# Kernel optimization log

Measured on AMD Instinct MI355X. Metric: run time of the kernel, lower is better.

## Reference

```python
import jax, jax.numpy as jnp
import numpy as np

N_NODES = 100_000
N_EDGES = 20_000   # hyperedges
NNZ = 2_000_000    # incidence pairs
F = 128
BN_EPS = 1e-5


def setup_inputs() -> dict:
    key = jax.random.key(0)
    ks = jax.random.split(key, 6)
    x_0 = jax.random.normal(ks[0], (N_NODES, F), dtype=jnp.float32)
    x_1 = jax.random.normal(ks[1], (N_EDGES, F), dtype=jnp.float32)
    node_idx = jax.random.randint(ks[2], (NNZ,), 0, N_NODES, dtype=jnp.int32)
    edge_idx = jax.random.randint(ks[3], (NNZ,), 0, N_EDGES, dtype=jnp.int32)
    W_nh = jax.random.normal(ks[4], (F, F), dtype=jnp.float32) / np.float32(np.sqrt(F))
    b_nh = jnp.zeros((F,), jnp.float32)
    W_en = jax.random.normal(ks[5], (F, 2 * F), dtype=jnp.float32) / np.float32(np.sqrt(2 * F))
    b_en = jnp.zeros((F,), jnp.float32)
    ones = jnp.ones((F,), jnp.float32)
    zeros = jnp.zeros((F,), jnp.float32)
    return {
        "x_0": x_0, "x_1": x_1, "node_idx": node_idx, "edge_idx": edge_idx,
        "W_nh": W_nh, "b_nh": b_nh, "W_en": W_en, "b_en": b_en,
        "bn0_gamma": ones, "bn0_beta": zeros, "bn0_mean": zeros, "bn0_var": ones,
        "bn1_gamma": ones, "bn1_beta": zeros, "bn1_mean": zeros, "bn1_var": ones,
    }


def _bn_eval(x, gamma, beta, mean, var):
    # BatchNorm1d in eval mode: normalize with running stats.
    return (x - mean) * (gamma * jax.lax.rsqrt(var + BN_EPS)) + beta


def reference(x_0, x_1, node_idx, edge_idx, W_nh, b_nh, W_en, b_en,
              bn0_gamma, bn0_beta, bn0_mean, bn0_var,
              bn1_gamma, bn1_beta, bn1_mean, bn1_var):
    # --- node -> hyperedge messenger ---
    # per-node message: sigmoid(Linear(x_0))  [n_nodes, F]
    node_messages = jax.nn.sigmoid(x_0 @ W_nh.T + b_nh)
    # gather over incidence list, scatter-sum onto hyperedges  [n_edges, F]
    node_msg_agg = jax.ops.segment_sum(node_messages[node_idx], edge_idx,
                                       num_segments=N_EDGES)

    # --- hyperedge -> node messenger ---
    # per-hyperedge message: sigmoid(Linear(cat(x_1, agg node msgs)))  [n_edges, F]
    he_messages = jax.nn.sigmoid(
        jnp.concatenate([x_1, node_msg_agg], axis=1) @ W_en.T + b_en)
    # gather per incidence, scatter-sum onto nodes  [n_nodes, F]
    he_msg_agg = jax.ops.segment_sum(he_messages[edge_idx], node_idx,
                                     num_segments=N_NODES)

    # --- updates (eval mode: feature dropout is identity) ---
    x0_out = jax.nn.sigmoid(
        _bn_eval(x_0, bn0_gamma, bn0_beta, bn0_mean, bn0_var) + he_msg_agg)
    x1_out = jax.nn.sigmoid(
        _bn_eval(x_1, bn1_gamma, bn1_beta, bn1_mean, bn1_var) + node_msg_agg)
    return (x0_out, x1_out)
```

## Files before the change

### kernel.cpp

```cpp
#include <hip/hip_runtime.h>
#include <hip/hip_bf16.h>
#include <math.h>

#define NNODES 100000
#define NEDGES 20000
#define NNZ_   2000000
#define FDIM   128
#define BN_EPS 1e-5f

#define NBUCK 256
#define CAP   9216
#define BPB_E 79
#define BPB_N 391
#define SH_E  17
#define SH_N  15

__device__ __forceinline__ float sigmoidf_(float x) {
    return 1.0f / (1.0f + __expf(-x));
}
__device__ __forceinline__ float bf2f(unsigned short u) {
    return __uint_as_float(((unsigned)u) << 16);
}
__device__ __forceinline__ unsigned short f2bf(float f) {
    __hip_bfloat16 h = __float2bfloat16(f);
    return *reinterpret_cast<unsigned short*>(&h);
}

__global__ __launch_bounds__(256) void transpose2(
    const float* __restrict__ W_nh, const float* __restrict__ W_en,
    float* __restrict__ WTnh, float* __restrict__ WTen)
{
    int idx = blockIdx.x * blockDim.x + threadIdx.x;
    if (idx < FDIM * FDIM) {
        int k = idx >> 7, c = idx & 127;
        WTnh[idx] = W_nh[c * FDIM + k];
    } else {
        int j = idx - FDIM * FDIM;
        if (j >= 2 * FDIM * FDIM) return;
        int k = j >> 7, c = j & 127;
        WTen[j] = W_en[c * 2 * FDIM + k];
    }
}

template<int K>
__global__ __launch_bounds__(256, 2) void gemm_sig_bf16(
    const float* __restrict__ A1, const float* __restrict__ A2,
    const float* __restrict__ WT, const float* __restrict__ bias,
    unsigned short* __restrict__ out)
{
    constexpr int BK = 64;
    constexpr int TM = 32;
    __shared__ float As[TM][BK + 4];
    __shared__ float Ws[BK][FDIM];
    const int tid  = threadIdx.x;
    const int row0 = blockIdx.x * TM;
    const int tcol = tid & 31;
    const int trow = tid >> 5;
    float acc[4][4] = {};

    for (int kk = 0; kk < K; kk += BK) {
        const float* Asrc = (kk < FDIM) ? A1 : A2;
        const int koff    = (kk < FDIM) ? kk : kk - FDIM;
        #pragma unroll
        for (int i = 0; i < 2; i++) {
            int l = tid + i * 256;
            int r = l >> 4, j = l & 15;
            float4 v = *(const float4*)(Asrc + (size_t)(row0 + r) * FDIM + koff + j * 4);
            *(float4*)&As[r][j * 4] = v;
        }
        #pragma unroll
        for (int i = 0; i < 8; i++) {
            int l = tid + i * 256;
            int k = l >> 5, j = l & 31;
            float4 v = *(const float4*)(WT + (size_t)(kk + k) * FDIM + j * 4);
            *(float4*)&Ws[k][j * 4] = v;
        }
        __syncthreads();
        #pragma unroll
        for (int k = 0; k < BK; k += 4) {
            float4 a[4];
            #pragma unroll
            for (int r = 0; r < 4; r++)
                a[r] = *(const float4*)&As[trow * 4 + r][k];
            #pragma unroll
            for (int kq = 0; kq < 4; kq++) {
                float4 w = *(const float4*)&Ws[k + kq][tcol * 4];
                #pragma unroll
                for (int r = 0; r < 4; r++) {
                    float av = (kq == 0) ? a[r].x : (kq == 1) ? a[r].y
                             : (kq == 2) ? a[r].z : a[r].w;
                    acc[r][0] += av * w.x;
                    acc[r][1] += av * w.y;
                    acc[r][2] += av * w.z;
                    acc[r][3] += av * w.w;
                }
            }
        }
        __syncthreads();
    }
    float4 bv = *(const float4*)(bias + tcol * 4);
    #pragma unroll
    for (int r = 0; r < 4; r++) {
        int row = row0 + trow * 4 + r;
        ushort4 o;
        o.x = f2bf(sigmoidf_(acc[r][0] + bv.x));
        o.y = f2bf(sigmoidf_(acc[r][1] + bv.y));
        o.z = f2bf(sigmoidf_(acc[r][2] + bv.z));
        o.w = f2bf(sigmoidf_(acc[r][3] + bv.w));
        *(ushort4*)(out + (size_t)row * FDIM + tcol * 4) = o;
    }
}

__global__ __launch_bounds__(1024) void bucket_scatter(
    const int* __restrict__ ni, const int* __restrict__ ei,
    unsigned* __restrict__ buck_e, unsigned* __restrict__ buck_n,
    int* __restrict__ gcur_e, int* __restrict__ gcur_n)
{
    __shared__ int lh_e[NBUCK], lh_n[NBUCK], lb_e[NBUCK], lb_n[NBUCK];
    const int t = threadIdx.x;
    if (t < NBUCK) { lh_e[t] = 0; lh_n[t] = 0; }
    __syncthreads();
    unsigned ent_e[4], ent_n[4];
    int be[4], bn[4], re[4], rn[4];
    const int base = blockIdx.x * 4096;
    #pragma unroll
    for (int j = 0; j < 4; j++) {
        int i = base + j * 1024 + t;
        if (i < NNZ_) {
            unsigned n = (unsigned)ni[i], e = (unsigned)ei[i];
            ent_e[j] = (e << SH_E) | n;  be[j] = (int)(e / BPB_E);
            ent_n[j] = (n << SH_N) | e;  bn[j] = (int)(n / BPB_N);
            re[j] = atomicAdd(&lh_e[be[j]], 1);
            rn[j] = atomicAdd(&lh_n[bn[j]], 1);
        } else { be[j] = -1; }
    }
    __syncthreads();
    if (t < NBUCK) {
        lb_e[t] = t * CAP + atomicAdd(&gcur_e[t], lh_e[t]);
        lb_n[t] = t * CAP + atomicAdd(&gcur_n[t], lh_n[t]);
    }
    __syncthreads();
    #pragma unroll
    for (int j = 0; j < 4; j++) {
        if (be[j] >= 0) {
            buck_e[(size_t)lb_e[be[j]] + re[j]] = ent_e[j];
            buck_n[(size_t)lb_n[bn[j]] + rn[j]] = ent_n[j];
        }
    }
}

__global__ __launch_bounds__(256) void bucket_bases(
    const int* __restrict__ gcur_e, const int* __restrict__ gcur_n,
    int* __restrict__ base_e, int* __restrict__ base_n)
{
    __shared__ int sh[NBUCK];
    int t = threadIdx.x;
    int v = gcur_e[t]; sh[t] = v; __syncthreads();
    for (int d = 1; d < NBUCK; d <<= 1) {
        int u = (t >= d) ? sh[t - d] : 0; __syncthreads();
        sh[t] += u; __syncthreads();
    }
    base_e[t] = sh[t] - v; __syncthreads();
    int v2 = gcur_n[t]; sh[t] = v2; __syncthreads();
    for (int d = 1; d < NBUCK; d <<= 1) {
        int u = (t >= d) ? sh[t - d] : 0; __syncthreads();
        sh[t] += u; __syncthreads();
    }
    base_n[t] = sh[t] - v2;
}

template<int BPB, int SH, unsigned MASK, int NBINS, typename OUT>
__device__ __forceinline__ void sort_bucket(
    const unsigned* __restrict__ region, int cnt, int gbase, int b0,
    OUT* __restrict__ csr, int* __restrict__ off)
{
    __shared__ unsigned lh[512];
    __shared__ unsigned lw[4];
    const int t = threadIdx.x;
    lh[t] = 0; lh[t + 256] = 0;
    __syncthreads();
    for (int i = t; i < cnt; i += 256) {
        int bin = (int)(region[i] >> SH) - b0;
        atomicAdd(&lh[bin], 1u);
    }
    __syncthreads();
    unsigned h0 = lh[2 * t], h1 = lh[2 * t + 1];
    unsigned s = h0 + h1, inc = s;
    const int lane = t & 63;
    #pragma unroll
    for (int d = 1; d <= 32; d <<= 1) {
        unsigned v = (unsigned)__shfl_up((int)inc, d, 64);
        if (lane >= d) inc += v;
    }
    if (lane == 63) lw[t >> 6] = inc;
    __syncthreads();
    unsigned pre = 0;
    #pragma unroll
    for (int w = 0; w < 4; w++) if (w < (t >> 6)) pre += lw[w];
    unsigned excl = pre + inc - s;
    unsigned c0 = (unsigned)gbase + excl;
    unsigned c1 = c0 + h0;
    lh[2 * t] = c0; lh[2 * t + 1] = c1;
    int i0 = 2 * t, i1 = 2 * t + 1;
    if (i0 <= BPB && b0 + i0 <= NBINS) off[b0 + i0] = (int)c0;
    if (i1 <= BPB && b0 + i1 <= NBINS) off[b0 + i1] = (int)c1;
    __syncthreads();
    for (int i = t; i < cnt; i += 256) {
        unsigned ent = region[i];
        int bin = (int)(ent >> SH) - b0;
        unsigned pos = atomicAdd(&lh[bin], 1u);
        csr[pos] = (OUT)(ent & MASK);
    }
}

__global__ __launch_bounds__(256) void bucket_sort(
    const unsigned* __restrict__ buck_e, const unsigned* __restrict__ buck_n,
    const int* __restrict__ gcur_e, const int* __restrict__ gcur_n,
    const int* __restrict__ base_e, const int* __restrict__ base_n,
    unsigned* __restrict__ csr_e, unsigned short* __restrict__ csr_n,
    int* __restrict__ off_e, int* __restrict__ off_n)
{
    int b = blockIdx.x & 255;
    if (blockIdx.x < 256)
        sort_bucket<BPB_E, SH_E, 0x1FFFFu, NEDGES, unsigned>(
            buck_e + (size_t)b * CAP, gcur_e[b], base_e[b], b * BPB_E, csr_e, off_e);
    else
        sort_bucket<BPB_N, SH_N, 0x7FFFu, NNODES, unsigned short>(
            buck_n + (size_t)b * CAP, gcur_n[b], base_n[b], b * BPB_N, csr_n, off_n);
}

template<typename IDX>
__global__ __launch_bounds__(256) void seg_sum_fin_bf16(
    const unsigned short* __restrict__ table, const IDX* __restrict__ csr,
    const int* __restrict__ off, const float* __restrict__ x,
    const float* __restrict__ g, const float* __restrict__ bb,
    const float* __restrict__ mm, const float* __restrict__ vv,
    float* __restrict__ agg_out, float* __restrict__ fin_out, int nseg)
{
    int gid = blockIdx.x * blockDim.x + threadIdx.x;
    int seg = gid >> 5;
    if (seg >= nseg) return;
    int q = (gid & 31) * 4;
    int i0 = off[seg], i1 = off[seg + 1];
    float4 acc = make_float4(0.f, 0.f, 0.f, 0.f);
    int i = i0;
    for (; i + 3 < i1; i += 4) {
        int r0 = (int)csr[i], r1 = (int)csr[i + 1];
        int r2 = (int)csr[i + 2], r3 = (int)csr[i + 3];
        ushort4 a0 = *(const ushort4*)(table + (size_t)r0 * FDIM + q);
        ushort4 a1 = *(const ushort4*)(table + (size_t)r1 * FDIM + q);
        ushort4 a2 = *(const ushort4*)(table + (size_t)r2 * FDIM + q);
        ushort4 a3 = *(const ushort4*)(table + (size_t)r3 * FDIM + q);
        acc.x += (bf2f(a0.x) + bf2f(a1.x)) + (bf2f(a2.x) + bf2f(a3.x));
        acc.y += (bf2f(a0.y) + bf2f(a1.y)) + (bf2f(a2.y) + bf2f(a3.y));
        acc.z += (bf2f(a0.z) + bf2f(a1.z)) + (bf2f(a2.z) + bf2f(a3.z));
        acc.w += (bf2f(a0.w) + bf2f(a1.w)) + (bf2f(a2.w) + bf2f(a3.w));
    }
    for (; i < i1; i++) {
        int r = (int)csr[i];
        ushort4 a = *(const ushort4*)(table + (size_t)r * FDIM + q);
        acc.x += bf2f(a.x); acc.y += bf2f(a.y);
        acc.z += bf2f(a.z); acc.w += bf2f(a.w);
    }
    if (agg_out)
        *(float4*)(agg_out + (size_t)seg * FDIM + q) = acc;
    if (fin_out) {
        float4 xv = *(const float4*)(x + (size_t)seg * FDIM + q);
        float4 gg = *(const float4*)(g + q);
        float4 bt = *(const float4*)(bb + q);
        float4 mn = *(const float4*)(mm + q);
        float4 vr = *(const float4*)(vv + q);
        float4 o;
        o.x = sigmoidf_((xv.x - mn.x) * (gg.x * rsqrtf(vr.x + BN_EPS)) + bt.x + acc.x);
        o.y = sigmoidf_((xv.y - mn.y) * (gg.y * rsqrtf(vr.y + BN_EPS)) + bt.y + acc.y);
        o.z = sigmoidf_((xv.z - mn.z) * (gg.z * rsqrtf(vr.z + BN_EPS)) + bt.z + acc.z);
        o.w = sigmoidf_((xv.w - mn.w) * (gg.w * rsqrtf(vr.w + BN_EPS)) + bt.w + acc.w);
        *(float4*)(fin_out + (size_t)seg * FDIM + q) = o;
    }
}

extern "C" void kernel_launch(void* const* d_in, const int* in_sizes, int n_in,
                              void* d_out, int out_size, void* d_ws, size_t ws_size,
                              hipStream_t stream)
{
    const float* x0       = (const float*)d_in[0];
    const float* x1       = (const float*)d_in[1];
    const int*   node_idx = (const int*)d_in[2];
    const int*   edge_idx = (const int*)d_in[3];
    const float* W_nh     = (const float*)d_in[4];
    const float* b_nh     = (const float*)d_in[5];
    const float* W_en     = (const float*)d_in[6];
    const float* b_en     = (const float*)d_in[7];
    const float* bn0g = (const float*)d_in[8];
    const float* bn0b = (const float*)d_in[9];
    const float* bn0m = (const float*)d_in[10];
    const float* bn0v = (const float*)d_in[11];
    const float* bn1g = (const float*)d_in[12];
    const float* bn1b = (const float*)d_in[13];
    const float* bn1m = (const float*)d_in[14];
    const float* bn1v = (const float*)d_in[15];

    float* ws = (float*)d_ws;
    float* B    = ws;
    float* WTnh = B + (size_t)NEDGES * FDIM;
    float* WTen = WTnh + FDIM * FDIM;
    unsigned short* A_bf = (unsigned short*)(WTen + 2 * FDIM * FDIM);
    unsigned short* D_bf = A_bf + (size_t)NNODES * FDIM;
    int* ip    = (int*)(D_bf + (size_t)NEDGES * FDIM);
    int* off_e = ip;
    int* off_n = off_e + 20004;
    unsigned* csr_e = (unsigned*)(off_n + 100004);
    unsigned short* csr_n = (unsigned short*)(csr_e + NNZ_);
    unsigned* buck_e = (unsigned*)(csr_n + NNZ_);
    unsigned* buck_n = buck_e + (size_t)NBUCK * CAP;
    int* gcur_e = (int*)(buck_n + (size_t)NBUCK * CAP);
    int* gcur_n = gcur_e + NBUCK;
    int* base_e = gcur_n + NBUCK;
    int* base_n = base_e + NBUCK;

    hipMemsetAsync(gcur_e, 0, 2 * NBUCK * sizeof(int), stream);
    bucket_scatter<<<(NNZ_ + 4095) / 4096, 1024, 0, stream>>>(
        node_idx, edge_idx, buck_e, buck_n, gcur_e, gcur_n);
    bucket_bases<<<1, 256, 0, stream>>>(gcur_e, gcur_n, base_e, base_n);
    bucket_sort<<<2 * NBUCK, 256, 0, stream>>>(buck_e, buck_n, gcur_e, gcur_n,
                                               base_e, base_n, csr_e, csr_n,
                                               off_e, off_n);

    transpose2<<<(3 * FDIM * FDIM + 255) / 256, 256, 0, stream>>>(W_nh, W_en, WTnh, WTen);

    float* out0 = (float*)d_out;
    float* out1 = out0 + (size_t)NNODES * FDIM;

    gemm_sig_bf16<128><<<NNODES / 32, 256, 0, stream>>>(x0, nullptr, WTnh, b_nh, A_bf);
    seg_sum_fin_bf16<unsigned><<<(NEDGES * 32 + 255) / 256, 256, 0, stream>>>(
        A_bf, csr_e, off_e, x1, bn1g, bn1b, bn1m, bn1v, B, out1, NEDGES);

    gemm_sig_bf16<256><<<NEDGES / 32, 256, 0, stream>>>(x1, B, WTen, b_en, D_bf);
    seg_sum_fin_bf16<unsigned short><<<(NNODES * 32 + 255) / 256, 256, 0, stream>>>(
        D_bf, csr_n, off_n, x0, bn0g, bn0b, bn0m, bn0v, nullptr, out0, NNODES);
}
```

Baseline: 423.5 us.

## Use bf16 MFMA for node GEMM and fold bucket prefix scan into sort

```diff
diff --git a/kernel.cpp b/kernel.cpp
--- a/kernel.cpp
+++ b/kernel.cpp
@@ -15,6 +15,9 @@
 #define SH_E  17
 #define SH_N  15
 
+typedef __attribute__((ext_vector_type(8))) short bf16x8_t;
+typedef __attribute__((ext_vector_type(4))) float f32x4_t;
+
 __device__ __forceinline__ float sigmoidf_(float x) {
     return 1.0f / (1.0f + __expf(-x));
 }
@@ -26,14 +29,13 @@
     return *reinterpret_cast<unsigned short*>(&h);
 }
 
-__global__ __launch_bounds__(256) void transpose2(
+__global__ __launch_bounds__(256) void prep_w(
     const float* __restrict__ W_nh, const float* __restrict__ W_en,
-    float* __restrict__ WTnh, float* __restrict__ WTen)
+    unsigned short* __restrict__ Wnh_bf, float* __restrict__ WTen)
 {
     int idx = blockIdx.x * blockDim.x + threadIdx.x;
     if (idx < FDIM * FDIM) {
-        int k = idx >> 7, c = idx & 127;
-        WTnh[idx] = W_nh[c * FDIM + k];
+        Wnh_bf[idx] = f2bf(W_nh[idx]);
     } else {
         int j = idx - FDIM * FDIM;
         if (j >= 2 * FDIM * FDIM) return;
@@ -42,22 +44,69 @@
     }
 }
 
-template<int K>
+__global__ __launch_bounds__(256) void gemm1_mfma(
+    const float* __restrict__ x0, const unsigned short* __restrict__ Wb,
+    const float* __restrict__ bias, unsigned short* __restrict__ out)
+{
+    __shared__ unsigned short As[32][FDIM + 8];
+    const int tid  = threadIdx.x;
+    const int row0 = blockIdx.x * 32;
+    {
+        int r = tid >> 3, c0 = (tid & 7) * 16;
+        const float* src = x0 + (size_t)(row0 + r) * FDIM + c0;
+        unsigned short* dst = &As[r][c0];
+        #pragma unroll
+        for (int i = 0; i < 4; i++) {
+            float4 v = *(const float4*)(src + i * 4);
+            dst[i * 4 + 0] = f2bf(v.x);
+            dst[i * 4 + 1] = f2bf(v.y);
+            dst[i * 4 + 2] = f2bf(v.z);
+            dst[i * 4 + 3] = f2bf(v.w);
+        }
+    }
+    __syncthreads();
+    const int wave  = tid >> 6;
+    const int lane  = tid & 63;
+    const int mhalf = wave & 1;
+    const int nhalf = wave >> 1;
+    const int lm    = lane & 15;
+    const int quad  = lane >> 4;
+    f32x4_t acc[4] = {};
+    #pragma unroll
+    for (int ks = 0; ks < 4; ks++) {
+        bf16x8_t a = *(const bf16x8_t*)&As[mhalf * 16 + lm][ks * 32 + quad * 8];
+        #pragma unroll
+        for (int nt = 0; nt < 4; nt++) {
+            int n = nhalf * 64 + nt * 16 + lm;
+            bf16x8_t b = *(const bf16x8_t*)(Wb + (size_t)n * FDIM + ks * 32 + quad * 8);
+            acc[nt] = __builtin_amdgcn_mfma_f32_16x16x32_bf16(a, b, acc[nt], 0, 0, 0);
+        }
+    }
+    const int mbase = row0 + mhalf * 16 + quad * 4;
+    #pragma unroll
+    for (int nt = 0; nt < 4; nt++) {
+        int n = nhalf * 64 + nt * 16 + lm;
+        float bv = bias[n];
+        #pragma unroll
+        for (int r2 = 0; r2 < 4; r2++) {
+            out[(size_t)(mbase + r2) * FDIM + n] = f2bf(sigmoidf_(acc[nt][r2] + bv));
+        }
+    }
+}
+
 __global__ __launch_bounds__(256, 2) void gemm_sig_bf16(
     const float* __restrict__ A1, const float* __restrict__ A2,
     const float* __restrict__ WT, const float* __restrict__ bias,
     unsigned short* __restrict__ out)
 {
-    constexpr int BK = 64;
-    constexpr int TM = 32;
-    __shared__ float As[TM][BK + 4];
+    constexpr int K = 256, BK = 64;
+    __shared__ float As[32][BK + 4];
     __shared__ float Ws[BK][FDIM];
     const int tid  = threadIdx.x;
-    const int row0 = blockIdx.x * TM;
+    const int row0 = blockIdx.x * 32;
     const int tcol = tid & 31;
     const int trow = tid >> 5;
     float acc[4][4] = {};
-
     for (int kk = 0; kk < K; kk += BK) {
         const float* Asrc = (kk < FDIM) ? A1 : A2;
         const int koff    = (kk < FDIM) ? kk : kk - FDIM;
@@ -149,26 +198,6 @@
     }
 }
 
-__global__ __launch_bounds__(256) void bucket_bases(
-    const int* __restrict__ gcur_e, const int* __restrict__ gcur_n,
-    int* __restrict__ base_e, int* __restrict__ base_n)
-{
-    __shared__ int sh[NBUCK];
-    int t = threadIdx.x;
-    int v = gcur_e[t]; sh[t] = v; __syncthreads();
-    for (int d = 1; d < NBUCK; d <<= 1) {
-        int u = (t >= d) ? sh[t - d] : 0; __syncthreads();
-        sh[t] += u; __syncthreads();
-    }
-    base_e[t] = sh[t] - v; __syncthreads();
-    int v2 = gcur_n[t]; sh[t] = v2; __syncthreads();
-    for (int d = 1; d < NBUCK; d <<= 1) {
-        int u = (t >= d) ? sh[t - d] : 0; __syncthreads();
-        sh[t] += u; __syncthreads();
-    }
-    base_n[t] = sh[t] - v2;
-}
-
 template<int BPB, int SH, unsigned MASK, int NBINS, typename OUT>
 __device__ __forceinline__ void sort_bucket(
     const unsigned* __restrict__ region, int cnt, int gbase, int b0,
@@ -216,17 +245,27 @@
 __global__ __launch_bounds__(256) void bucket_sort(
     const unsigned* __restrict__ buck_e, const unsigned* __restrict__ buck_n,
     const int* __restrict__ gcur_e, const int* __restrict__ gcur_n,
-    const int* __restrict__ base_e, const int* __restrict__ base_n,
     unsigned* __restrict__ csr_e, unsigned short* __restrict__ csr_n,
     int* __restrict__ off_e, int* __restrict__ off_n)
 {
-    int b = blockIdx.x & 255;
+    const int b = blockIdx.x & 255;
+    const int* gc = (blockIdx.x < 256) ? gcur_e : gcur_n;
+    __shared__ int ws4[4];
+    const int t = threadIdx.x;
+    int v = (t < b) ? gc[t] : 0;
+    #pragma unroll
+    for (int d = 32; d > 0; d >>= 1) v += __shfl_down(v, d, 64);
+    if ((t & 63) == 0) ws4[t >> 6] = v;
+    __syncthreads();
+    const int gbase = ws4[0] + ws4[1] + ws4[2] + ws4[3];
+    const int cnt = gc[b];
+    __syncthreads();
     if (blockIdx.x < 256)
         sort_bucket<BPB_E, SH_E, 0x1FFFFu, NEDGES, unsigned>(
-            buck_e + (size_t)b * CAP, gcur_e[b], base_e[b], b * BPB_E, csr_e, off_e);
+            buck_e + (size_t)b * CAP, cnt, gbase, b * BPB_E, csr_e, off_e);
     else
         sort_bucket<BPB_N, SH_N, 0x7FFFu, NNODES, unsigned short>(
-            buck_n + (size_t)b * CAP, gcur_n[b], base_n[b], b * BPB_N, csr_n, off_n);
+            buck_n + (size_t)b * CAP, cnt, gbase, b * BPB_N, csr_n, off_n);
 }
 
 template<typename IDX>
@@ -302,9 +341,9 @@
 
     float* ws = (float*)d_ws;
     float* B    = ws;
-    float* WTnh = B + (size_t)NEDGES * FDIM;
-    float* WTen = WTnh + FDIM * FDIM;
-    unsigned short* A_bf = (unsigned short*)(WTen + 2 * FDIM * FDIM);
+    float* WTen = B + (size_t)NEDGES * FDIM;
+    unsigned short* Wnh_bf = (unsigned short*)(WTen + 2 * FDIM * FDIM);
+    unsigned short* A_bf = Wnh_bf + FDIM * FDIM;
     unsigned short* D_bf = A_bf + (size_t)NNODES * FDIM;
     int* ip    = (int*)(D_bf + (size_t)NEDGES * FDIM);
     int* off_e = ip;
@@ -315,27 +354,23 @@
     unsigned* buck_n = buck_e + (size_t)NBUCK * CAP;
     int* gcur_e = (int*)(buck_n + (size_t)NBUCK * CAP);
     int* gcur_n = gcur_e + NBUCK;
-    int* base_e = gcur_n + NBUCK;
-    int* base_n = base_e + NBUCK;
 
     hipMemsetAsync(gcur_e, 0, 2 * NBUCK * sizeof(int), stream);
     bucket_scatter<<<(NNZ_ + 4095) / 4096, 1024, 0, stream>>>(
         node_idx, edge_idx, buck_e, buck_n, gcur_e, gcur_n);
-    bucket_bases<<<1, 256, 0, stream>>>(gcur_e, gcur_n, base_e, base_n);
     bucket_sort<<<2 * NBUCK, 256, 0, stream>>>(buck_e, buck_n, gcur_e, gcur_n,
-                                               base_e, base_n, csr_e, csr_n,
-                                               off_e, off_n);
-
-    transpose2<<<(3 * FDIM * FDIM + 255) / 256, 256, 0, stream>>>(W_nh, W_en, WTnh, WTen);
+                                               csr_e, csr_n, off_e, off_n);
+
+    prep_w<<<(3 * FDIM * FDIM + 255) / 256, 256, 0, stream>>>(W_nh, W_en, Wnh_bf, WTen);
 
     float* out0 = (float*)d_out;
     float* out1 = out0 + (size_t)NNODES * FDIM;
 
-    gemm_sig_bf16<128><<<NNODES / 32, 256, 0, stream>>>(x0, nullptr, WTnh, b_nh, A_bf);
+    gemm1_mfma<<<NNODES / 32, 256, 0, stream>>>(x0, Wnh_bf, b_nh, A_bf);
     seg_sum_fin_bf16<unsigned><<<(NEDGES * 32 + 255) / 256, 256, 0, stream>>>(
         A_bf, csr_e, off_e, x1, bn1g, bn1b, bn1m, bn1v, B, out1, NEDGES);
 
-    gemm_sig_bf16<256><<<NEDGES / 32, 256, 0, stream>>>(x1, B, WTen, b_en, D_bf);
+    gemm_sig_bf16<<<NEDGES / 32, 256, 0, stream>>>(x1, B, WTen, b_en, D_bf);
     seg_sum_fin_bf16<unsigned short><<<(NNODES * 32 + 255) / 256, 256, 0, stream>>>(
         D_bf, csr_n, off_n, x0, bn0g, bn0b, bn0m, bn0v, nullptr, out0, NNODES);
 }
```

Result: faster. 404.6 us (-4.5%).
